# Kernel tuning notes

Measured on AMD Instinct MI355X. Metric: run time of the kernel, lower is better.

The kernel has to match this reference:

```python
import jax, jax.numpy as jnp
import numpy as np
import math

B, T, D, K, V = 8, 2048, 512, 512, 512


def setup_inputs() -> dict:
    key = jax.random.key(0)
    ks = jax.random.split(key, 4)
    minibatch = jax.random.normal(ks[0], (B, T, D), dtype=jnp.float32)
    # nn.Linear weights are [out, in]; biases [out]
    Wk = jax.random.normal(ks[1], (K, D), dtype=jnp.float32) * 0.02
    bk = jnp.zeros((K,), dtype=jnp.float32)
    Wq = jax.random.normal(ks[2], (K, D), dtype=jnp.float32) * 0.02
    bq = jnp.zeros((K,), dtype=jnp.float32)
    Wv = jax.random.normal(ks[3], (V, D), dtype=jnp.float32) * 0.02
    bv = jnp.zeros((V,), dtype=jnp.float32)
    return {"minibatch": minibatch, "Wk": Wk, "bk": bk, "Wq": Wq, "bq": bq, "Wv": Wv, "bv": bv}


def reference(minibatch, Wk, bk, Wq, bq, Wv, bv):
    k_size = Wk.shape[0]
    sqrt_k = math.sqrt(k_size)
    keys = jnp.einsum('btd,kd->btk', minibatch, Wk) + bk
    queries = jnp.einsum('btd,kd->btk', minibatch, Wq) + bq
    values = jnp.einsum('btd,vd->btv', minibatch, Wv) + bv
    # logits[b, t, s] = q_t . k_s
    logits = jnp.einsum('btk,bsk->bts', queries, keys)
    seq = minibatch.shape[1]
    # upper triangle (s > t) masked to -inf, matching np.triu(..., k=1)
    mask = jnp.triu(jnp.ones((seq, seq), dtype=bool), k=1)
    logits = jnp.where(mask[None, :, :], -jnp.inf, logits)
    # NOTE: original softmaxes over dim=1 (the query axis), then divides by sqrt(k)
    probs = jax.nn.softmax(logits, axis=1) / sqrt_k
    read = jnp.einsum('bts,bsv->btv', probs, values)
    return minibatch + read
```

## Files before the change

kernel.cpp:

```cpp
#include <hip/hip_runtime.h>


typedef __attribute__((ext_vector_type(4))) float f32x4;
typedef __attribute__((ext_vector_type(8))) short s16x8;
typedef __attribute__((ext_vector_type(4))) short s16x4;

#define SQRTK  22.627416997969522f

__device__ __forceinline__ short f2bf(float f) {
    union { float f; unsigned int i; } c; c.f = f;
    unsigned int x = c.i;
    return (short)((x + 0x7fffu + ((x >> 16) & 1u)) >> 16);
}
__device__ __forceinline__ void gll16(const void* g, void* l) {
    __builtin_amdgcn_global_load_lds(
        (const __attribute__((address_space(1))) void*)g,
        (__attribute__((address_space(3))) void*)l, 16, 0, 0);
}

__global__ __launch_bounds__(256) void k_cast(
    const float* __restrict__ in, unsigned short* __restrict__ out, int n4)
{
    int i = blockIdx.x * 256 + threadIdx.x;
    if (i >= n4) return;
    f32x4 v = *(const f32x4*)(in + (size_t)i * 4);
    s16x4 o;
#pragma unroll
    for (int j = 0; j < 4; ++j) o[j] = f2bf(v[j]);
    *(s16x4*)(out + (size_t)i * 4) = o;
}

__global__ __launch_bounds__(256) void k_castw(
    const float* __restrict__ q, const float* __restrict__ k, const float* __restrict__ v,
    unsigned short* __restrict__ oqk, unsigned short* __restrict__ ov)
{
    int i = blockIdx.x * 256 + threadIdx.x;
    const float* src; unsigned short* dst; int j;
    if (i < 65536)       { src = q; dst = oqk; j = i; }
    else if (i < 131072) { src = k; dst = oqk + 262144; j = i - 65536; }
    else                 { src = v; dst = ov; j = i - 131072; }
    f32x4 w = *(const f32x4*)(src + (size_t)j * 4);
    s16x4 o;
#pragma unroll
    for (int jj = 0; jj < 4; ++jj) o[jj] = f2bf(w[jj]);
    *(s16x4*)(dst + (size_t)j * 4) = o;
}

__global__ __launch_bounds__(256) void k_projqk(
    const unsigned short* __restrict__ Xb,
    const unsigned short* __restrict__ Wqk,
    const float* __restrict__ bq, const float* __restrict__ bk,
    unsigned short* __restrict__ C)
{
    __shared__ short la[2][2][128][32];
    __shared__ short lb[2][2][128][32];
    const int tid  = threadIdx.x;
    const int wave = tid >> 6, lane = tid & 63;
    const int wr = (wave >> 1) * 64, wc = (wave & 1) * 64;
    const int m0 = blockIdx.x * 128, n0 = blockIdx.y * 128;
    const int r0 = tid >> 2, c0 = (tid & 3) * 8;
    const int wvb = wave * 1024;
    const int frl = lane & 15, kb = (lane >> 4) * 8, rg4 = (lane >> 4) * 4;
    f32x4 acc[4][4] = {};

#define QK_STAGE(BUF, K0) { \
    _Pragma("unroll") for (int h = 0; h < 2; ++h) { \
        char* pa_ = (char*)(&la[BUF][h][0][0]) + wvb; \
        char* pb_ = (char*)(&lb[BUF][h][0][0]) + wvb; \
        gll16(Xb  + (size_t)(m0 + r0) * 512 + (K0) + h * 32 + c0, pa_); \
        gll16(Xb  + (size_t)(m0 + r0 + 64) * 512 + (K0) + h * 32 + c0, pa_ + 4096); \
        gll16(Wqk + (size_t)(n0 + r0) * 512 + (K0) + h * 32 + c0, pb_); \
        gll16(Wqk + (size_t)(n0 + r0 + 64) * 512 + (K0) + h * 32 + c0, pb_ + 4096); } }

    QK_STAGE(0, 0);
    __syncthreads();
    for (int ks = 0; ks < 8; ++ks) {
        const int cur = ks & 1;
        if (ks < 7) QK_STAGE(cur ^ 1, (ks + 1) * 64);
#pragma unroll
        for (int h = 0; h < 2; ++h) {
            s16x8 af[4], bfr[4];
#pragma unroll
            for (int i = 0; i < 4; ++i) af[i]  = *(const s16x8*)(&la[cur][h][wr + i * 16 + frl][kb]);
#pragma unroll
            for (int i = 0; i < 4; ++i) bfr[i] = *(const s16x8*)(&lb[cur][h][wc + i * 16 + frl][kb]);
#pragma unroll
            for (int mi = 0; mi < 4; ++mi)
#pragma unroll
                for (int ni = 0; ni < 4; ++ni)
                    acc[mi][ni] = __builtin_amdgcn_mfma_f32_16x16x32_bf16(af[mi], bfr[ni], acc[mi][ni], 0, 0, 0);
        }
        __syncthreads();
    }
#undef QK_STAGE
#pragma unroll
    for (int mi = 0; mi < 4; ++mi)
#pragma unroll
        for (int ni = 0; ni < 4; ++ni) {
            int col = n0 + wc + ni * 16 + frl;
            float bv = (col < 512) ? bq[col] : bk[col - 512];
#pragma unroll
            for (int r = 0; r < 4; ++r) {
                int row = m0 + wr + mi * 16 + rg4 + r;
                C[(size_t)row * 1024 + col] = f2bf(acc[mi][ni][r] + bv);
            }
        }
}

__global__ __launch_bounds__(256) void k_projv(
    const unsigned short* __restrict__ Wv,
    const unsigned short* __restrict__ Xb,
    const float* __restrict__ bv,
    const float* __restrict__ ft,
    unsigned short* __restrict__ C)
{
    __shared__ short la[2][128][32];
    __shared__ short lb[2][128][32];
    const int tid  = threadIdx.x;
    const int wave = tid >> 6, lane = tid & 63;
    const int wr = (wave >> 1) * 64, wc = (wave & 1) * 64;
    const int m0 = blockIdx.x * 128, n0 = blockIdx.y * 128;
    const int r0 = tid >> 2, c0 = (tid & 3) * 8;
    const int wvb = wave * 1024;
    const int frl = lane & 15, kb = (lane >> 4) * 8, rg4 = (lane >> 4) * 4;
    f32x4 acc[4][4] = {};

#define PV_STAGE(BUF, K0) { \
    char* pa_ = (char*)(&la[BUF][0][0]) + wvb; \
    char* pb_ = (char*)(&lb[BUF][0][0]) + wvb; \
    gll16(Wv + (size_t)(m0 + r0) * 512 + (K0) + c0, pa_); \
    gll16(Wv + (size_t)(m0 + r0 + 64) * 512 + (K0) + c0, pa_ + 4096); \
    gll16(Xb + (size_t)(n0 + r0) * 512 + (K0) + c0, pb_); \
    gll16(Xb + (size_t)(n0 + r0 + 64) * 512 + (K0) + c0, pb_ + 4096); }

    PV_STAGE(0, 0);
    __syncthreads();
    for (int ks = 0; ks < 16; ++ks) {
        const int cur = ks & 1;
        if (ks < 15) PV_STAGE(cur ^ 1, (ks + 1) * 32);
        s16x8 af[4], bfr[4];
#pragma unroll
        for (int i = 0; i < 4; ++i) af[i]  = *(const s16x8*)(&la[cur][wr + i * 16 + frl][kb]);
#pragma unroll
        for (int i = 0; i < 4; ++i) bfr[i] = *(const s16x8*)(&lb[cur][wc + i * 16 + frl][kb]);
#pragma unroll
        for (int mi = 0; mi < 4; ++mi)
#pragma unroll
            for (int ni = 0; ni < 4; ++ni)
                acc[mi][ni] = __builtin_amdgcn_mfma_f32_16x16x32_bf16(af[mi], bfr[ni], acc[mi][ni], 0, 0, 0);
        __syncthreads();
    }
#undef PV_STAGE
#pragma unroll
    for (int mi = 0; mi < 4; ++mi)
#pragma unroll
        for (int ni = 0; ni < 4; ++ni) {
            int col = n0 + wc + ni * 16 + frl;
            float fs = ft[col];
#pragma unroll
            for (int r = 0; r < 4; ++r) {
                int row = m0 + wr + mi * 16 + rg4 + r;
                C[(size_t)row * 16384 + col] = f2bf((acc[mi][ni][r] + bv[row]) * fs);
            }
        }
}

__global__ __launch_bounds__(256) void k_logits(
    const unsigned short* __restrict__ QK,
    unsigned short* __restrict__ Pc,
    float* __restrict__ pz)
{
    const int n = blockIdx.x;
    const int b = n & 7;
    const int p = n >> 3;
    int tt = (int)((sqrtf(8.f * p + 1.f) - 1.f) * 0.5f);
    while ((tt + 1) * (tt + 2) / 2 <= p) ++tt;
    while (tt * (tt + 1) / 2 > p) --tt;
    const int st = p - tt * (tt + 1) / 2;
    const int t0 = tt * 128, s0 = st * 128;

    const unsigned short* A  = QK + (size_t)b * 2048 * 1024;
    const unsigned short* Bt = QK + (size_t)b * 2048 * 1024 + 512;
    unsigned short* Pb = Pc + (size_t)b * 2048 * 2048;

    __shared__ short la[2][2][128][32];
    __shared__ short lb[2][2][128][32];
    __shared__ float sz[2][128];
    const int tid  = threadIdx.x;
    const int wave = tid >> 6, lane = tid & 63;
    const int wr = (wave >> 1) * 64, wc = (wave & 1) * 64;
    const int r0 = tid >> 2, c0 = (tid & 3) * 8;
    const int wvb = wave * 1024;
    const int frl = lane & 15, kb = (lane >> 4) * 8, rg4 = (lane >> 4) * 4;
    f32x4 acc[4][4] = {};

#define LG_STAGE(BUF, K0) { \
    _Pragma("unroll") for (int h = 0; h < 2; ++h) { \
        char* pa_ = (char*)(&la[BUF][h][0][0]) + wvb; \
        char* pb_ = (char*)(&lb[BUF][h][0][0]) + wvb; \
        gll16(A  + (size_t)(t0 + r0) * 1024 + (K0) + h * 32 + c0, pa_); \
        gll16(A  + (size_t)(t0 + r0 + 64) * 1024 + (K0) + h * 32 + c0, pa_ + 4096); \
        gll16(Bt + (size_t)(s0 + r0) * 1024 + (K0) + h * 32 + c0, pb_); \
        gll16(Bt + (size_t)(s0 + r0 + 64) * 1024 + (K0) + h * 32 + c0, pb_ + 4096); } }

    LG_STAGE(0, 0);
    __syncthreads();
    for (int ks = 0; ks < 8; ++ks) {
        const int cur = ks & 1;
        if (ks < 7) LG_STAGE(cur ^ 1, (ks + 1) * 64);
#pragma unroll
        for (int h = 0; h < 2; ++h) {
            s16x8 af[4], bfr[4];
#pragma unroll
            for (int i = 0; i < 4; ++i) af[i]  = *(const s16x8*)(&la[cur][h][wr + i * 16 + frl][kb]);
#pragma unroll
            for (int i = 0; i < 4; ++i) bfr[i] = *(const s16x8*)(&lb[cur][h][wc + i * 16 + frl][kb]);
#pragma unroll
            for (int mi = 0; mi < 4; ++mi)
#pragma unroll
                for (int ni = 0; ni < 4; ++ni)
                    acc[mi][ni] = __builtin_amdgcn_mfma_f32_16x16x32_bf16(af[mi], bfr[ni], acc[mi][ni], 0, 0, 0);
        }
        __syncthreads();
    }
#undef LG_STAGE

    float cz[4];
#pragma unroll
    for (int ni = 0; ni < 4; ++ni) {
        const int colg = s0 + wc + ni * 16 + frl;
        float zl = 0.f;
#pragma unroll
        for (int mi = 0; mi < 4; ++mi)
#pragma unroll
            for (int r = 0; r < 4; ++r) {
                int row = t0 + wr + mi * 16 + rg4 + r;
                float e = (colg <= row) ? __expf(acc[mi][ni][r]) : 0.f;
                acc[mi][ni][r] = e;
                zl += e;
            }
        zl += __shfl_xor(zl, 16);
        zl += __shfl_xor(zl, 32);
        cz[ni] = zl;
    }
    if (lane < 16) {
#pragma unroll
        for (int ni = 0; ni < 4; ++ni)
            sz[wr >> 6][wc + ni * 16 + lane] = cz[ni];
    }
    __syncthreads();
    if (tid < 128)
        pz[(b * 16 + tt) * 2048 + s0 + tid] = sz[0][tid] + sz[1][tid];
#pragma unroll
    for (int ni = 0; ni < 4; ++ni) {
        const int colg = s0 + wc + ni * 16 + frl;
#pragma unroll
        for (int mi = 0; mi < 4; ++mi)
#pragma unroll
            for (int r = 0; r < 4; ++r) {
                int row = t0 + wr + mi * 16 + rg4 + r;
                Pb[(size_t)row * 2048 + colg] = f2bf(acc[mi][ni][r]);
            }
    }
}

__global__ __launch_bounds__(256) void k_stats2(
    const float* __restrict__ pz, float* __restrict__ ft)
{
    const int i = blockIdx.x * 256 + threadIdx.x;
    const int b = i >> 11, s = i & 2047;
    float Z = 0.f;
    for (int tc = s >> 7; tc < 16; ++tc) Z += pz[(b * 16 + tc) * 2048 + s];
    ft[i] = 1.0f / (Z * SQRTK);
}

__global__ __launch_bounds__(256) void k_out(
    const unsigned short* __restrict__ Pc,
    const unsigned short* __restrict__ Vs,
    const float* __restrict__ X,
    float* __restrict__ Y)
{
    __shared__ short la[2][2][128][32];
    __shared__ short lb[2][2][128][32];
    const int n  = blockIdx.x;
    const int tt = 15 - (n >> 5);
    const int b  = n & 7;
    const int v  = (n >> 3) & 3;
    const int t0 = tt * 128, v0 = v * 128;
    const unsigned short* Pb = Pc + (size_t)b * 2048 * 2048;
    const int tid  = threadIdx.x;
    const int wave = tid >> 6, lane = tid & 63;
    const int wr = (wave >> 1) * 64, wc = (wave & 1) * 64;
    const int frl = lane & 15, kb = (lane >> 4) * 8, rg4 = (lane >> 4) * 4;
    const int r0 = tid >> 2, c0 = (tid & 3) * 8;
    const int wvb = wave * 1024;

    f32x4 acc[4][4] = {};
    const int nit = (tt + 1) * 2;

#define OUT_STAGE(BUF, IT) { \
    int sb = (IT) * 64; \
    _Pragma("unroll") for (int h = 0; h < 2; ++h) { \
        char* pa_ = (char*)(&la[BUF][h][0][0]) + wvb; \
        char* pb_ = (char*)(&lb[BUF][h][0][0]) + wvb; \
        gll16(Pb + (size_t)(t0 + r0) * 2048 + sb + h * 32 + c0, pa_); \
        gll16(Pb + (size_t)(t0 + r0 + 64) * 2048 + sb + h * 32 + c0, pa_ + 4096); \
        gll16(Vs + (size_t)(v0 + r0) * 16384 + b * 2048 + sb + h * 32 + c0, pb_); \
        gll16(Vs + (size_t)(v0 + r0 + 64) * 16384 + b * 2048 + sb + h * 32 + c0, pb_ + 4096); } }

    OUT_STAGE(0, 0);
    __syncthreads();
    for (int it = 0; it < nit; ++it) {
        const int cur = it & 1;
        if (it + 1 < nit) OUT_STAGE(cur ^ 1, it + 1);
#pragma unroll
        for (int h = 0; h < 2; ++h) {
            s16x8 af[4], bfr[4];
#pragma unroll
            for (int i = 0; i < 4; ++i) af[i]  = *(const s16x8*)(&la[cur][h][wr + i * 16 + frl][kb]);
#pragma unroll
            for (int i = 0; i < 4; ++i) bfr[i] = *(const s16x8*)(&lb[cur][h][wc + i * 16 + frl][kb]);
#pragma unroll
            for (int mi = 0; mi < 4; ++mi)
#pragma unroll
                for (int ni = 0; ni < 4; ++ni)
                    acc[mi][ni] = __builtin_amdgcn_mfma_f32_16x16x32_bf16(af[mi], bfr[ni], acc[mi][ni], 0, 0, 0);
        }
        __syncthreads();
    }
#undef OUT_STAGE

#pragma unroll
    for (int mi = 0; mi < 4; ++mi)
#pragma unroll
        for (int ni = 0; ni < 4; ++ni) {
            int col = v0 + wc + ni * 16 + frl;
#pragma unroll
            for (int r = 0; r < 4; ++r) {
                int row = t0 + wr + mi * 16 + rg4 + r;
                size_t o = ((size_t)b * 2048 + row) * 512 + col;
                Y[o] = acc[mi][ni][r] + X[o];
            }
        }
}

extern "C" void kernel_launch(void* const* d_in, const int* in_sizes, int n_in,
                              void* d_out, int out_size, void* d_ws, size_t ws_size,
                              hipStream_t stream) {
    const float* Xf  = (const float*)d_in[0];
    const float* Wkf = (const float*)d_in[1];
    const float* bkf = (const float*)d_in[2];
    const float* Wqf = (const float*)d_in[3];
    const float* bqf = (const float*)d_in[4];
    const float* Wvf = (const float*)d_in[5];
    const float* bvf = (const float*)d_in[6];
    float* Y = (float*)d_out;
    char* ws = (char*)d_ws;

    float*          pz   = (float*)(ws);
    float*          ftab = (float*)(ws + 2097152);
    unsigned short* Wqkb = (unsigned short*)(ws + 4194304);
    unsigned short* Wvb  = (unsigned short*)(ws + 5242880);
    unsigned short* Xb   = (unsigned short*)(ws + 6291456);
    unsigned short* QKb  = (unsigned short*)(ws + 23068672);
    unsigned short* Vs   = (unsigned short*)(ws + 56623104);
    unsigned short* Pc   = (unsigned short*)(ws + 73400320);

    dim3 blk(256);
    k_cast<<<dim3(8192), blk, 0, stream>>>(Xf, Xb, 2097152);
    k_castw<<<dim3(768), blk, 0, stream>>>(Wqf, Wkf, Wvf, Wqkb, Wvb);
    k_projqk<<<dim3(128, 8), blk, 0, stream>>>(Xb, Wqkb, bqf, bkf, QKb);
    k_logits<<<dim3(1088), blk, 0, stream>>>(QKb, Pc, pz);
    k_stats2<<<dim3(64), blk, 0, stream>>>(pz, ftab);
    k_projv<<<dim3(4, 128), blk, 0, stream>>>(Wvb, Xb, bvf, ftab, Vs);
    k_out<<<dim3(512), blk, 0, stream>>>(Pc, Vs, Xf, Y);
}
```

Measured before the change: 137.5 us.

## Merge cast kernels, fold column-sum normalization into projv, interleave k_out tile order

The X cast and the weight casts now run as one kernel, and the separate k_stats2 launch is removed. The per-column normalization sum from pz is now computed inside the k_projv epilogue. k_out's block mapping now alternates light and heavy causal tiles so work per scheduling wave is more even. This cuts two launches and a small global table round trip. In exchange, every k_projv block recomputes up to 16 pz loads per output column, which repeats reads across the 4 row-tile blocks.

```diff
diff --git a/kernel.cpp b/kernel.cpp
--- a/kernel.cpp
+++ b/kernel.cpp
@@ -18,27 +18,21 @@
         (__attribute__((address_space(3))) void*)l, 16, 0, 0);
 }
 
-__global__ __launch_bounds__(256) void k_cast(
-    const float* __restrict__ in, unsigned short* __restrict__ out, int n4)
-{
-    int i = blockIdx.x * 256 + threadIdx.x;
-    if (i >= n4) return;
-    f32x4 v = *(const f32x4*)(in + (size_t)i * 4);
-    s16x4 o;
-#pragma unroll
-    for (int j = 0; j < 4; ++j) o[j] = f2bf(v[j]);
-    *(s16x4*)(out + (size_t)i * 4) = o;
-}
-
-__global__ __launch_bounds__(256) void k_castw(
-    const float* __restrict__ q, const float* __restrict__ k, const float* __restrict__ v,
-    unsigned short* __restrict__ oqk, unsigned short* __restrict__ ov)
+__global__ __launch_bounds__(256) void k_casts(
+    const float* __restrict__ x, const float* __restrict__ q,
+    const float* __restrict__ k, const float* __restrict__ v,
+    unsigned short* __restrict__ ox, unsigned short* __restrict__ oqk,
+    unsigned short* __restrict__ ov)
 {
     int i = blockIdx.x * 256 + threadIdx.x;
     const float* src; unsigned short* dst; int j;
-    if (i < 65536)       { src = q; dst = oqk; j = i; }
-    else if (i < 131072) { src = k; dst = oqk + 262144; j = i - 65536; }
-    else                 { src = v; dst = ov; j = i - 131072; }
+    if (i < 2097152)      { src = x; dst = ox; j = i; }
+    else {
+        j = i - 2097152;
+        if (j < 65536)       { src = q; dst = oqk; }
+        else if (j < 131072) { src = k; dst = oqk + 262144; j -= 65536; }
+        else                 { src = v; dst = ov; j -= 131072; }
+    }
     f32x4 w = *(const f32x4*)(src + (size_t)j * 4);
     s16x4 o;
 #pragma unroll
@@ -111,7 +105,7 @@
     const unsigned short* __restrict__ Wv,
     const unsigned short* __restrict__ Xb,
     const float* __restrict__ bv,
-    const float* __restrict__ ft,
+    const float* __restrict__ pz,
     unsigned short* __restrict__ C)
 {
     __shared__ short la[2][128][32];
@@ -156,7 +150,11 @@
 #pragma unroll
         for (int ni = 0; ni < 4; ++ni) {
             int col = n0 + wc + ni * 16 + frl;
-            float fs = ft[col];
+            const int bb = col >> 11, ss = col & 2047;
+            float Z = 0.f;
+            for (int tc = ss >> 7; tc < 16; ++tc)
+                Z += pz[(bb * 16 + tc) * 2048 + ss];
+            const float fs = 1.0f / (Z * SQRTK);
 #pragma unroll
             for (int r = 0; r < 4; ++r) {
                 int row = m0 + wr + mi * 16 + rg4 + r;
@@ -264,16 +262,6 @@
     }
 }
 
-__global__ __launch_bounds__(256) void k_stats2(
-    const float* __restrict__ pz, float* __restrict__ ft)
-{
-    const int i = blockIdx.x * 256 + threadIdx.x;
-    const int b = i >> 11, s = i & 2047;
-    float Z = 0.f;
-    for (int tc = s >> 7; tc < 16; ++tc) Z += pz[(b * 16 + tc) * 2048 + s];
-    ft[i] = 1.0f / (Z * SQRTK);
-}
-
 __global__ __launch_bounds__(256) void k_out(
     const unsigned short* __restrict__ Pc,
     const unsigned short* __restrict__ Vs,
@@ -283,9 +271,11 @@
     __shared__ short la[2][2][128][32];
     __shared__ short lb[2][2][128][32];
     const int n  = blockIdx.x;
-    const int tt = 15 - (n >> 5);
     const int b  = n & 7;
-    const int v  = (n >> 3) & 3;
+    const int h  = (n >> 3) & 1;
+    const int q  = (n >> 4) & 7;
+    const int v  = (n >> 7) & 3;
+    const int tt = h ? (15 - q) : q;
     const int t0 = tt * 128, v0 = v * 128;
     const unsigned short* Pb = Pc + (size_t)b * 2048 * 2048;
     const int tid  = threadIdx.x;
@@ -300,13 +290,13 @@
 
 #define OUT_STAGE(BUF, IT) { \
     int sb = (IT) * 64; \
-    _Pragma("unroll") for (int h = 0; h < 2; ++h) { \
-        char* pa_ = (char*)(&la[BUF][h][0][0]) + wvb; \
-        char* pb_ = (char*)(&lb[BUF][h][0][0]) + wvb; \
-        gll16(Pb + (size_t)(t0 + r0) * 2048 + sb + h * 32 + c0, pa_); \
-        gll16(Pb + (size_t)(t0 + r0 + 64) * 2048 + sb + h * 32 + c0, pa_ + 4096); \
-        gll16(Vs + (size_t)(v0 + r0) * 16384 + b * 2048 + sb + h * 32 + c0, pb_); \
-        gll16(Vs + (size_t)(v0 + r0 + 64) * 16384 + b * 2048 + sb + h * 32 + c0, pb_ + 4096); } }
+    _Pragma("unroll") for (int hh = 0; hh < 2; ++hh) { \
+        char* pa_ = (char*)(&la[BUF][hh][0][0]) + wvb; \
+        char* pb_ = (char*)(&lb[BUF][hh][0][0]) + wvb; \
+        gll16(Pb + (size_t)(t0 + r0) * 2048 + sb + hh * 32 + c0, pa_); \
+        gll16(Pb + (size_t)(t0 + r0 + 64) * 2048 + sb + hh * 32 + c0, pa_ + 4096); \
+        gll16(Vs + (size_t)(v0 + r0) * 16384 + b * 2048 + sb + hh * 32 + c0, pb_); \
+        gll16(Vs + (size_t)(v0 + r0 + 64) * 16384 + b * 2048 + sb + hh * 32 + c0, pb_ + 4096); } }
 
     OUT_STAGE(0, 0);
     __syncthreads();
@@ -314,12 +304,12 @@
         const int cur = it & 1;
         if (it + 1 < nit) OUT_STAGE(cur ^ 1, it + 1);
 #pragma unroll
-        for (int h = 0; h < 2; ++h) {
+        for (int hh = 0; hh < 2; ++hh) {
             s16x8 af[4], bfr[4];
 #pragma unroll
-            for (int i = 0; i < 4; ++i) af[i]  = *(const s16x8*)(&la[cur][h][wr + i * 16 + frl][kb]);
-#pragma unroll
-            for (int i = 0; i < 4; ++i) bfr[i] = *(const s16x8*)(&lb[cur][h][wc + i * 16 + frl][kb]);
+            for (int i = 0; i < 4; ++i) af[i]  = *(const s16x8*)(&la[cur][hh][wr + i * 16 + frl][kb]);
+#pragma unroll
+            for (int i = 0; i < 4; ++i) bfr[i] = *(const s16x8*)(&lb[cur][hh][wc + i * 16 + frl][kb]);
 #pragma unroll
             for (int mi = 0; mi < 4; ++mi)
 #pragma unroll
@@ -358,7 +348,6 @@
     char* ws = (char*)d_ws;
 
     float*          pz   = (float*)(ws);
-    float*          ftab = (float*)(ws + 2097152);
     unsigned short* Wqkb = (unsigned short*)(ws + 4194304);
     unsigned short* Wvb  = (unsigned short*)(ws + 5242880);
     unsigned short* Xb   = (unsigned short*)(ws + 6291456);
@@ -367,11 +356,9 @@
     unsigned short* Pc   = (unsigned short*)(ws + 73400320);
 
     dim3 blk(256);
-    k_cast<<<dim3(8192), blk, 0, stream>>>(Xf, Xb, 2097152);
-    k_castw<<<dim3(768), blk, 0, stream>>>(Wqf, Wkf, Wvf, Wqkb, Wvb);
+    k_casts<<<dim3(8960), blk, 0, stream>>>(Xf, Wqf, Wkf, Wvf, Xb, Wqkb, Wvb);
     k_projqk<<<dim3(128, 8), blk, 0, stream>>>(Xb, Wqkb, bqf, bkf, QKb);
     k_logits<<<dim3(1088), blk, 0, stream>>>(QKb, Pc, pz);
-    k_stats2<<<dim3(64), blk, 0, stream>>>(pz, ftab);
-    k_projv<<<dim3(4, 128), blk, 0, stream>>>(Wvb, Xb, bvf, ftab, Vs);
+    k_projv<<<dim3(4, 128), blk, 0, stream>>>(Wvb, Xb, bvf, pz, Vs);
     k_out<<<dim3(512), blk, 0, stream>>>(Pc, Vs, Xf, Y);
 }
```

Result: slower. 176.4 us (+28.3%).
